# Kernel tuning notes

Measured on AMD Instinct MI355X. Metric: run time of the kernel, lower is better.

Reference implementation:

```python
import jax, jax.numpy as jnp
import numpy as np
import math

D_MODEL = 2048
K = 64
W = 512              # window_size
STRIDE = W // 2      # = 256
EMA_ALPHA = 0.9
N_RETRIEVE = 8
EPS = 1e-12


def _build_cheby(k, w):
    # cheby_mat[k, n] = cos(k * arccos(t_n)), t_n = cos(pi*(2n+1)/(2w))
    ns = np.arange(w, dtype=np.float64)
    t = np.cos(np.pi * (2 * ns + 1) / (2 * w))
    ks = np.arange(k, dtype=np.float64)
    return jnp.asarray(np.cos(ks[:, None] * np.arccos(t)[None, :]), dtype=jnp.float32)


def setup_inputs() -> dict:
    key = jax.random.key(0)
    ks = jax.random.split(key, 5)
    B, S = 2, 8192
    scan_out = jax.random.normal(ks[0], (B, S, D_MODEL), dtype=jnp.float32)
    buf = jax.random.normal(ks[1], (W, D_MODEL), dtype=jnp.float32)  # pre-filled circular buffer
    # unit-modulus random-phase complex roles: r_k[d] = exp(i*theta)
    phases = jax.random.uniform(ks[2], (K, D_MODEL), dtype=jnp.float32) * (2.0 * math.pi)
    roles_real = jnp.cos(phases)
    roles_imag = jnp.sin(phases)
    w_bands = 1.0 / (jnp.arange(K, dtype=jnp.float32) + 1.0)  # w_init = 1/(k+1)
    retrieve_proj_w = jax.random.normal(ks[3], (D_MODEL, D_MODEL), dtype=jnp.float32) * 0.02
    inject_gate = jnp.zeros((1,), dtype=jnp.float32)
    cheby_mat = _build_cheby(K, W)
    return dict(scan_out=scan_out, buf=buf, roles_real=roles_real, roles_imag=roles_imag,
                w_bands=w_bands, retrieve_proj_w=retrieve_proj_w, inject_gate=inject_gate,
                cheby_mat=cheby_mat)


def reference(scan_out, buf, roles_real, roles_imag, w_bands, retrieve_proj_w, inject_gate, cheby_mat):
    S = scan_out.shape[1]
    h_mean = scan_out.mean(axis=0)                      # [S, D] batch-mean like torch code
    n_chunks = S // STRIDE
    chunks = h_mean.reshape(n_chunks, STRIDE, D_MODEL)  # each chunk triggers one bind

    init = (buf, jnp.int32(0),
            jnp.zeros((K, D_MODEL), jnp.float32),   # c_past
            jnp.zeros((D_MODEL,), jnp.float32),     # V_mem_real
            jnp.zeros((D_MODEL,), jnp.float32),     # V_mem_imag
            jnp.zeros((K,), jnp.float32),           # _coeff_norms (EMA)
            jnp.zeros((K,), jnp.float32))           # spectral_delta

    def step(carry, chunk):
        b, pos, c_past, vr, vi, cnorms, _ = carry
        # circular-buffer write of `stride` tokens starting at pos
        b = jax.lax.dynamic_update_slice(b, chunk, (pos, 0))
        pos = (pos + STRIDE) % W
        order = (jnp.arange(W, dtype=jnp.int32) + pos) % W   # oldest-first reorder
        data = b[order]                                      # [W, D]
        # Chebyshev coefficients: c = (2/W) * cheby_mat @ data, c0 halved
        coeffs = (2.0 / W) * (cheby_mat @ data)              # [K, D]
        coeffs = coeffs.at[0].multiply(0.5)
        # HRR-normalized bind into holographic memory via EMA
        norms = jnp.maximum(jnp.linalg.norm(coeffs, axis=-1, keepdims=True), EPS)
        cn = coeffs / norms
        cnorms = EMA_ALPHA * cnorms + (1.0 - EMA_ALPHA) * norms[:, 0]
        vr = EMA_ALPHA * vr + (1.0 - EMA_ALPHA) * (cn * roles_real).sum(axis=0)
        vi = EMA_ALPHA * vi + (1.0 - EMA_ALPHA) * (cn * roles_imag).sum(axis=0)
        # spectral delta vs previous window's coefficients
        delta = jnp.linalg.norm(coeffs - c_past, axis=-1)    # [K]
        return (b, pos, coeffs, vr, vi, cnorms, delta), None

    (b, pos, c_now, vr, vi, cnorms, delta), _ = jax.lax.scan(step, init, chunks)

    # retrieve: unbind top-J bands by spectral delta, denormalize, weight, project
    _, top = jax.lax.top_k(delta, N_RETRIEVE)                # [J]
    rr = roles_real[top]
    ri = roles_imag[top]
    retrieved = (vr[None, :] * rr + vi[None, :] * ri) * jnp.maximum(cnorms[top], EPS)[:, None]  # [J, D]
    weights = jax.nn.softplus(w_bands[top])                  # [J]
    ctx = (weights[:, None] * retrieved).sum(axis=0)         # [D]
    out = (ctx @ retrieve_proj_w.T) * jax.nn.sigmoid(inject_gate[0])  # [D]
    return out, delta, vr, vi
```

## Files before the change

kernel.cpp:

```cpp
#include <hip/hip_runtime.h>
#include <math.h>

#define D_MODEL 2048
#define KB_ 64
#define NCHUNK 32

typedef __bf16 bf16;
typedef __attribute__((ext_vector_type(8))) __bf16 bf16x8;
typedef __attribute__((ext_vector_type(4))) __bf16 bf16x4;
typedef __attribute__((ext_vector_type(4))) float f32x4;

#define OFF_COEFFS 0
#define OFF_NSQ    (32 * 64 * 2048)
#define OFF_NORMS  (OFF_NSQ + 32 * 64 * 32)
#define OFF_PARTR  (OFF_NORMS + 2048)
#define OFF_PARTI  (OFF_PARTR + 32 * 2048)
#define OFF_CTX    (OFF_PARTI + 32 * 2048)
#define OFF_CHEB2  (OFF_CTX + 2048)

__global__ __launch_bounds__(256) void k0_prep(
    const float* __restrict__ cheby, bf16* __restrict__ cheb2)
{
  int flat = blockIdx.x * 256 + threadIdx.x;
  cheb2[flat] = (bf16)cheby[flat];
}

__global__ __launch_bounds__(256, 4) void k1_mfma(
    const float* __restrict__ scan, const float* __restrict__ buf,
    const bf16* __restrict__ cheb2, float* __restrict__ coeffs,
    float* __restrict__ nsq_part)
{
  __shared__ bf16 Bs[2][64 * 72];

  const int t = threadIdx.x;
  const int dt = blockIdx.x;
  const int c  = blockIdx.y;
  const int w = t >> 6, lane = t & 63;
  const int quad = lane >> 4, r16 = lane & 15;
  const int d0 = dt * 64;
  const int n0 = (t >> 4) * 4;
  const int d4 = (t & 15) * 4;
  const float* scan1 = scan + 8192 * 2048;

  f32x4 acc[4];
#pragma unroll
  for (int tn = 0; tn < 4; ++tn) acc[tn] = (f32x4){0.f, 0.f, 0.f, 0.f};

  float vv[4][4], vvn[4][4];

  auto loadB = [&](int nb, float (*v)[4]) {
    if (c == 0 && nb < 4) {
      const float* bp = buf + (256 + nb * 64 + n0) * 2048 + d0 + d4;
#pragma unroll
      for (int i = 0; i < 4; ++i) {
        float4 x = *(const float4*)(bp + i * 2048);
        v[i][0] = x.x; v[i][1] = x.y; v[i][2] = x.z; v[i][3] = x.w;
      }
    } else {
      int gbase = ((c - 1) * 256 + nb * 64 + n0) * 2048 + d0 + d4;
#pragma unroll
      for (int i = 0; i < 4; ++i) {
        float4 a = *(const float4*)(scan + gbase + i * 2048);
        float4 b = *(const float4*)(scan1 + gbase + i * 2048);
        v[i][0] = 0.5f * (a.x + b.x); v[i][1] = 0.5f * (a.y + b.y);
        v[i][2] = 0.5f * (a.z + b.z); v[i][3] = 0.5f * (a.w + b.w);
      }
    }
  };

  loadB(0, vv);
  for (int nb = 0; nb < 8; ++nb) {
    bf16* Bw = Bs[nb & 1];
#pragma unroll
    for (int x = 0; x < 4; ++x) {
      bf16x4 e = {(bf16)vv[0][x], (bf16)vv[1][x], (bf16)vv[2][x], (bf16)vv[3][x]};
      *(bf16x4*)(Bw + (d4 + x) * 72 + n0) = e;
    }
    __syncthreads();
    if (nb < 7) loadB(nb + 1, vvn);
    const bf16* abase = cheb2 + (w * 16 + r16) * 512 + nb * 64 + quad * 8;
    bf16x8 a0 = *(const bf16x8*)(abase);
    bf16x8 a1 = *(const bf16x8*)(abase + 32);
#pragma unroll
    for (int ks = 0; ks < 2; ++ks) {
      bf16x8 a = ks ? a1 : a0;
#pragma unroll
      for (int tn = 0; tn < 4; ++tn) {
        bf16x8 bfr = *(const bf16x8*)(Bw + (tn * 16 + r16) * 72 + ks * 32 + quad * 8);
        acc[tn] = __builtin_amdgcn_mfma_f32_16x16x32_bf16(a, bfr, acc[tn], 0, 0, 0);
      }
    }
#pragma unroll
    for (int i = 0; i < 4; ++i)
#pragma unroll
      for (int x = 0; x < 4; ++x) vv[i][x] = vvn[i][x];
  }

  const float scale = 2.0f / 512.0f;
  float sq[4] = {0.f, 0.f, 0.f, 0.f};
#pragma unroll
  for (int tn = 0; tn < 4; ++tn) {
#pragma unroll
    for (int rr = 0; rr < 4; ++rr) {
      int band = w * 16 + quad * 4 + rr;
      float sc = (band == 0) ? scale * 0.5f : scale;
      float v = acc[tn][rr] * sc;
      coeffs[(c * 64 + band) * 2048 + d0 + tn * 16 + r16] = v;
      sq[rr] += v * v;
    }
  }
#pragma unroll
  for (int off = 8; off > 0; off >>= 1) {
#pragma unroll
    for (int rr = 0; rr < 4; ++rr) sq[rr] += __shfl_down(sq[rr], off);
  }
  if (r16 == 0) {
#pragma unroll
    for (int rr = 0; rr < 4; ++rr)
      nsq_part[(c * 64 + w * 16 + quad * 4 + rr) * 32 + dt] = sq[rr];
  }
}

__global__ __launch_bounds__(256) void k3_bind(
    const float* __restrict__ coeffs, const float* __restrict__ nsq_part,
    const float* __restrict__ rr, const float* __restrict__ ri,
    float* __restrict__ part_r, float* __restrict__ part_i,
    float* __restrict__ norms, float* __restrict__ dout)
{
  const int tid = threadIdx.x;
  const int c = blockIdx.y;

  if (blockIdx.x == 2) {
    __shared__ float red[4];
#pragma unroll
    for (int kk = 0; kk < 2; ++kk) {
      int k = c + kk * 32;
      const float* p1 = coeffs + (31 * 64 + k) * 2048;
      const float* p0 = coeffs + (30 * 64 + k) * 2048;
      float s = 0.f;
#pragma unroll
      for (int i = 0; i < 2; ++i) {
        float4 a = *(const float4*)(p1 + tid * 4 + i * 1024);
        float4 b = *(const float4*)(p0 + tid * 4 + i * 1024);
        float x = a.x - b.x, y = a.y - b.y, z = a.z - b.z, ww = a.w - b.w;
        s += x * x + y * y + z * z + ww * ww;
      }
      for (int o = 32; o > 0; o >>= 1) s += __shfl_down(s, o, 64);
      if ((tid & 63) == 0) red[tid >> 6] = s;
      __syncthreads();
      if (tid == 0) dout[D_MODEL + k] = sqrtf(red[0] + red[1] + red[2] + red[3]);
      __syncthreads();
    }
    return;
  }

  __shared__ float inv_s[64];
  if (tid < 64) {
    float s = 0.f;
#pragma unroll
    for (int dtl = 0; dtl < 32; ++dtl) s += nsq_part[(c * 64 + tid) * 32 + dtl];
    float nrm = fmaxf(sqrtf(s), 1e-12f);
    inv_s[tid] = 1.0f / nrm;
    if (blockIdx.x == 0) norms[c * 64 + tid] = nrm;
  }
  __syncthreads();
  const int d4 = (blockIdx.x * 256 + tid) * 4;
  const float wc = 0.1f * powf(0.9f, (float)(31 - c));
  float4 ar = make_float4(0.f, 0.f, 0.f, 0.f);
  float4 ai = make_float4(0.f, 0.f, 0.f, 0.f);
  for (int k = 0; k < KB_; ++k) {
    float4 cf = *(const float4*)(coeffs + (c * 64 + k) * 2048 + d4);
    float inv = inv_s[k];
    float4 r = *(const float4*)(rr + k * D_MODEL + d4);
    float4 im = *(const float4*)(ri + k * D_MODEL + d4);
    float cx = cf.x * inv, cy = cf.y * inv, cz = cf.z * inv, cw = cf.w * inv;
    ar.x += cx * r.x; ar.y += cy * r.y; ar.z += cz * r.z; ar.w += cw * r.w;
    ai.x += cx * im.x; ai.y += cy * im.y; ai.z += cz * im.z; ai.w += cw * im.w;
  }
  *(float4*)(part_r + c * D_MODEL + d4) =
      make_float4(wc * ar.x, wc * ar.y, wc * ar.z, wc * ar.w);
  *(float4*)(part_i + c * D_MODEL + d4) =
      make_float4(wc * ai.x, wc * ai.y, wc * ai.z, wc * ai.w);
}

__global__ __launch_bounds__(256) void k4_ctx(
    const float* __restrict__ norms, const float* __restrict__ part_r,
    const float* __restrict__ part_i, const float* __restrict__ rr,
    const float* __restrict__ ri, const float* __restrict__ wbands,
    float* __restrict__ dout, float* __restrict__ ctx)
{
  __shared__ float cn_s[64];
  __shared__ int top_s[8];
  __shared__ float wgt_s[8];
  const int tid = threadIdx.x;
  const int d = blockIdx.x * 256 + tid;
  if (tid < 64) {
    float s = 0.f;
    for (int c = 0; c < NCHUNK; ++c) s = 0.9f * s + 0.1f * norms[c * 64 + tid];
    cn_s[tid] = fmaxf(s, 1e-12f);
  }
  __syncthreads();
  if (tid == 0) {
    unsigned long long taken = 0ULL;
    for (int jj = 0; jj < 8; ++jj) {
      float best = -1.f;
      int bi = 0;
      for (int k = 0; k < 64; ++k) {
        float dv = dout[D_MODEL + k];
        if (!((taken >> k) & 1ULL) && dv > best) { best = dv; bi = k; }
      }
      taken |= (1ULL << bi);
      top_s[jj] = bi;
      wgt_s[jj] = log1pf(expf(wbands[bi]));
    }
  }
  __syncthreads();
  float sr = 0.f, si = 0.f;
  for (int c = 0; c < NCHUNK; ++c) {
    sr += part_r[c * D_MODEL + d];
    si += part_i[c * D_MODEL + d];
  }
  dout[D_MODEL + KB_ + d] = sr;
  dout[D_MODEL + KB_ + D_MODEL + d] = si;
  float cx = 0.f;
#pragma unroll
  for (int jj = 0; jj < 8; ++jj) {
    int k = top_s[jj];
    cx += wgt_s[jj] * (sr * rr[k * D_MODEL + d] + si * ri[k * D_MODEL + d]) * cn_s[k];
  }
  ctx[d] = cx;
}

__global__ __launch_bounds__(256) void k5b_gemv(
    const float* __restrict__ Wp, const float* __restrict__ ctx,
    const float* __restrict__ gate, float* __restrict__ dout)
{
  const int tid = threadIdx.x;
  const int lane = tid & 63;
  const int w = tid >> 6;
  const int row = blockIdx.x * 4 + w;
  const float* p = Wp + row * D_MODEL;
  float s = 0.f;
#pragma unroll
  for (int i = 0; i < 8; ++i) {
    int e = lane * 4 + i * 256;
    float4 wv = *(const float4*)(p + e);
    float4 cv = *(const float4*)(ctx + e);
    s += wv.x * cv.x + wv.y * cv.y + wv.z * cv.z + wv.w * cv.w;
  }
  for (int o = 32; o > 0; o >>= 1) s += __shfl_down(s, o, 64);
  if (lane == 0) {
    float sig = 1.f / (1.f + expf(-gate[0]));
    dout[row] = s * sig;
  }
}

extern "C" void kernel_launch(void* const* d_in, const int* in_sizes, int n_in,
                              void* d_out, int out_size, void* d_ws, size_t ws_size,
                              hipStream_t stream) {
  const float* scan  = (const float*)d_in[0];
  const float* buf   = (const float*)d_in[1];
  const float* rr    = (const float*)d_in[2];
  const float* ri    = (const float*)d_in[3];
  const float* wb    = (const float*)d_in[4];
  const float* Wp    = (const float*)d_in[5];
  const float* gate  = (const float*)d_in[6];
  const float* cheby = (const float*)d_in[7];
  float* out = (float*)d_out;
  float* ws = (float*)d_ws;

  float* coeffs   = ws + OFF_COEFFS;
  float* nsq_part = ws + OFF_NSQ;
  float* norms    = ws + OFF_NORMS;
  float* part_r   = ws + OFF_PARTR;
  float* part_i   = ws + OFF_PARTI;
  float* ctx      = ws + OFF_CTX;
  bf16*  cheb2    = (bf16*)(ws + OFF_CHEB2);

  k0_prep<<<128, 256, 0, stream>>>(cheby, cheb2);
  k1_mfma<<<dim3(32, 32), 256, 0, stream>>>(scan, buf, cheb2, coeffs, nsq_part);
  k3_bind<<<dim3(3, NCHUNK), 256, 0, stream>>>(coeffs, nsq_part, rr, ri,
                                               part_r, part_i, norms, out);
  k4_ctx<<<8, 256, 0, stream>>>(norms, part_r, part_i, rr, ri, wb, out, ctx);
  k5b_gemv<<<512, 256, 0, stream>>>(Wp, ctx, gate, out);
}
```

Measured before the change: 321.5 us.

## Share overlapping window chunks across window pairs in Chebyshev MFMA kernel

Each block now computes two adjacent windows over a 32-wide d-tile. The overlapping 256-token half is loaded once and fed to both windows' accumulators, so global reads of scan (which are averaged across the batch) drop from 8 to 6 slices per window-pair half. The grid changes to 64x16, the nsq partials widen to 64 d-tiles, and the LDS double buffer is removed in favour of a single buffer with an extra barrier. The cost is less load/compute overlap and the loss of the explicit prefetch.

```diff
diff --git a/kernel.cpp b/kernel.cpp
--- a/kernel.cpp
+++ b/kernel.cpp
@@ -7,12 +7,12 @@
 
 typedef __bf16 bf16;
 typedef __attribute__((ext_vector_type(8))) __bf16 bf16x8;
-typedef __attribute__((ext_vector_type(4))) __bf16 bf16x4;
+typedef __attribute__((ext_vector_type(2))) __bf16 bf16x2;
 typedef __attribute__((ext_vector_type(4))) float f32x4;
 
 #define OFF_COEFFS 0
 #define OFF_NSQ    (32 * 64 * 2048)
-#define OFF_NORMS  (OFF_NSQ + 32 * 64 * 32)
+#define OFF_NORMS  (OFF_NSQ + 32 * 64 * 64)
 #define OFF_PARTR  (OFF_NORMS + 2048)
 #define OFF_PARTI  (OFF_PARTR + 32 * 2048)
 #define OFF_CTX    (OFF_PARTI + 32 * 2048)
@@ -25,99 +25,108 @@
   cheb2[flat] = (bf16)cheby[flat];
 }
 
-__global__ __launch_bounds__(256, 4) void k1_mfma(
+__global__ __launch_bounds__(256) void k1_mfma(
     const float* __restrict__ scan, const float* __restrict__ buf,
     const bf16* __restrict__ cheb2, float* __restrict__ coeffs,
     float* __restrict__ nsq_part)
 {
-  __shared__ bf16 Bs[2][64 * 72];
+  __shared__ bf16 Bs[32 * 72];
 
   const int t = threadIdx.x;
   const int dt = blockIdx.x;
-  const int c  = blockIdx.y;
+  const int p  = blockIdx.y;
   const int w = t >> 6, lane = t & 63;
   const int quad = lane >> 4, r16 = lane & 15;
-  const int d0 = dt * 64;
-  const int n0 = (t >> 4) * 4;
-  const int d4 = (t & 15) * 4;
+  const int d0 = dt * 32;
+  const int n0 = (t >> 3) * 2;
+  const int d4 = (t & 7) * 4;
   const float* scan1 = scan + 8192 * 2048;
 
-  f32x4 acc[4];
-#pragma unroll
-  for (int tn = 0; tn < 4; ++tn) acc[tn] = (f32x4){0.f, 0.f, 0.f, 0.f};
-
-  float vv[4][4], vvn[4][4];
-
-  auto loadB = [&](int nb, float (*v)[4]) {
-    if (c == 0 && nb < 4) {
-      const float* bp = buf + (256 + nb * 64 + n0) * 2048 + d0 + d4;
-#pragma unroll
-      for (int i = 0; i < 4; ++i) {
+  f32x4 acc[2][2];
+#pragma unroll
+  for (int a = 0; a < 2; ++a)
+#pragma unroll
+    for (int b = 0; b < 2; ++b) acc[a][b] = (f32x4){0.f, 0.f, 0.f, 0.f};
+
+  for (int sl = 0; sl < 12; ++sl) {
+    const int q = sl & 3;
+    float vv[2][4];
+    if (p == 0 && sl < 4) {
+      const float* bp = buf + (256 + sl * 64 + n0) * 2048 + d0 + d4;
+#pragma unroll
+      for (int i = 0; i < 2; ++i) {
         float4 x = *(const float4*)(bp + i * 2048);
-        v[i][0] = x.x; v[i][1] = x.y; v[i][2] = x.z; v[i][3] = x.w;
+        vv[i][0] = x.x; vv[i][1] = x.y; vv[i][2] = x.z; vv[i][3] = x.w;
       }
     } else {
-      int gbase = ((c - 1) * 256 + nb * 64 + n0) * 2048 + d0 + d4;
-#pragma unroll
-      for (int i = 0; i < 4; ++i) {
+      const int jc = 2 * p - 1 + (sl >> 2);
+      const int gbase = (jc * 256 + q * 64 + n0) * 2048 + d0 + d4;
+#pragma unroll
+      for (int i = 0; i < 2; ++i) {
         float4 a = *(const float4*)(scan + gbase + i * 2048);
         float4 b = *(const float4*)(scan1 + gbase + i * 2048);
-        v[i][0] = 0.5f * (a.x + b.x); v[i][1] = 0.5f * (a.y + b.y);
-        v[i][2] = 0.5f * (a.z + b.z); v[i][3] = 0.5f * (a.w + b.w);
-      }
-    }
-  };
-
-  loadB(0, vv);
-  for (int nb = 0; nb < 8; ++nb) {
-    bf16* Bw = Bs[nb & 1];
+        vv[i][0] = 0.5f * (a.x + b.x); vv[i][1] = 0.5f * (a.y + b.y);
+        vv[i][2] = 0.5f * (a.z + b.z); vv[i][3] = 0.5f * (a.w + b.w);
+      }
+    }
+    __syncthreads();
 #pragma unroll
     for (int x = 0; x < 4; ++x) {
-      bf16x4 e = {(bf16)vv[0][x], (bf16)vv[1][x], (bf16)vv[2][x], (bf16)vv[3][x]};
-      *(bf16x4*)(Bw + (d4 + x) * 72 + n0) = e;
+      bf16x2 e = {(bf16)vv[0][x], (bf16)vv[1][x]};
+      *(bf16x2*)(Bs + (d4 + x) * 72 + n0) = e;
     }
     __syncthreads();
-    if (nb < 7) loadB(nb + 1, vvn);
-    const bf16* abase = cheb2 + (w * 16 + r16) * 512 + nb * 64 + quad * 8;
-    bf16x8 a0 = *(const bf16x8*)(abase);
-    bf16x8 a1 = *(const bf16x8*)(abase + 32);
+
+    const bool wa = (sl < 8), wb = (sl >= 4);
+    const int colA = sl * 64, colB = (sl - 4) * 64;
+    const int arow = (w * 16 + r16) * 512;
 #pragma unroll
     for (int ks = 0; ks < 2; ++ks) {
-      bf16x8 a = ks ? a1 : a0;
-#pragma unroll
-      for (int tn = 0; tn < 4; ++tn) {
-        bf16x8 bfr = *(const bf16x8*)(Bw + (tn * 16 + r16) * 72 + ks * 32 + quad * 8);
-        acc[tn] = __builtin_amdgcn_mfma_f32_16x16x32_bf16(a, bfr, acc[tn], 0, 0, 0);
-      }
-    }
-#pragma unroll
-    for (int i = 0; i < 4; ++i)
-#pragma unroll
-      for (int x = 0; x < 4; ++x) vv[i][x] = vvn[i][x];
+      bf16x8 bfr[2];
+#pragma unroll
+      for (int tn = 0; tn < 2; ++tn)
+        bfr[tn] = *(const bf16x8*)(Bs + (tn * 16 + r16) * 72 + ks * 32 + quad * 8);
+      if (wa) {
+        bf16x8 a = *(const bf16x8*)(cheb2 + arow + colA + ks * 32 + quad * 8);
+#pragma unroll
+        for (int tn = 0; tn < 2; ++tn)
+          acc[0][tn] = __builtin_amdgcn_mfma_f32_16x16x32_bf16(a, bfr[tn], acc[0][tn], 0, 0, 0);
+      }
+      if (wb) {
+        bf16x8 a = *(const bf16x8*)(cheb2 + arow + colB + ks * 32 + quad * 8);
+#pragma unroll
+        for (int tn = 0; tn < 2; ++tn)
+          acc[1][tn] = __builtin_amdgcn_mfma_f32_16x16x32_bf16(a, bfr[tn], acc[1][tn], 0, 0, 0);
+      }
+    }
   }
 
   const float scale = 2.0f / 512.0f;
-  float sq[4] = {0.f, 0.f, 0.f, 0.f};
-#pragma unroll
-  for (int tn = 0; tn < 4; ++tn) {
-#pragma unroll
-    for (int rr = 0; rr < 4; ++rr) {
-      int band = w * 16 + quad * 4 + rr;
-      float sc = (band == 0) ? scale * 0.5f : scale;
-      float v = acc[tn][rr] * sc;
-      coeffs[(c * 64 + band) * 2048 + d0 + tn * 16 + r16] = v;
-      sq[rr] += v * v;
-    }
-  }
-#pragma unroll
-  for (int off = 8; off > 0; off >>= 1) {
-#pragma unroll
-    for (int rr = 0; rr < 4; ++rr) sq[rr] += __shfl_down(sq[rr], off);
-  }
-  if (r16 == 0) {
-#pragma unroll
-    for (int rr = 0; rr < 4; ++rr)
-      nsq_part[(c * 64 + w * 16 + quad * 4 + rr) * 32 + dt] = sq[rr];
+#pragma unroll
+  for (int win = 0; win < 2; ++win) {
+    const int c = 2 * p + win;
+    float sq[4] = {0.f, 0.f, 0.f, 0.f};
+#pragma unroll
+    for (int tn = 0; tn < 2; ++tn) {
+#pragma unroll
+      for (int rr = 0; rr < 4; ++rr) {
+        int band = w * 16 + quad * 4 + rr;
+        float sc = (band == 0) ? scale * 0.5f : scale;
+        float v = acc[win][tn][rr] * sc;
+        coeffs[(c * 64 + band) * 2048 + d0 + tn * 16 + r16] = v;
+        sq[rr] += v * v;
+      }
+    }
+#pragma unroll
+    for (int off = 8; off > 0; off >>= 1) {
+#pragma unroll
+      for (int rr = 0; rr < 4; ++rr) sq[rr] += __shfl_down(sq[rr], off);
+    }
+    if (r16 == 0) {
+#pragma unroll
+      for (int rr = 0; rr < 4; ++rr)
+        nsq_part[(c * 64 + w * 16 + quad * 4 + rr) * 64 + dt] = sq[rr];
+    }
   }
 }
 
@@ -158,7 +167,7 @@
   if (tid < 64) {
     float s = 0.f;
 #pragma unroll
-    for (int dtl = 0; dtl < 32; ++dtl) s += nsq_part[(c * 64 + tid) * 32 + dtl];
+    for (int dtl = 0; dtl < 64; ++dtl) s += nsq_part[(c * 64 + tid) * 64 + dtl];
     float nrm = fmaxf(sqrtf(s), 1e-12f);
     inv_s[tid] = 1.0f / nrm;
     if (blockIdx.x == 0) norms[c * 64 + tid] = nrm;
@@ -278,7 +287,7 @@
   bf16*  cheb2    = (bf16*)(ws + OFF_CHEB2);
 
   k0_prep<<<128, 256, 0, stream>>>(cheby, cheb2);
-  k1_mfma<<<dim3(32, 32), 256, 0, stream>>>(scan, buf, cheb2, coeffs, nsq_part);
+  k1_mfma<<<dim3(64, 16), 256, 0, stream>>>(scan, buf, cheb2, coeffs, nsq_part);
   k3_bind<<<dim3(3, NCHUNK), 256, 0, stream>>>(coeffs, nsq_part, rr, ri,
                                                part_r, part_i, norms, out);
   k4_ctx<<<8, 256, 0, stream>>>(norms, part_r, part_i, rr, ri, wb, out, ctx);
```

Result: no change. 322.5 us (+0.3%).

## Fuse all stages into one cooperative persistent kernel with grid syncs

Applied to the files above, without the earlier changes.

Adds a cooperative kernel that runs the bf16 conversion, the Chebyshev MFMA projection, the bind/delta reduction, the context build and the GEMV as phases separated by grid-wide syncs, launched with 512 blocks. The intent is to remove per-launch overhead and the gaps between the five kernels. The MFMA phase processes 1024 tiles in a grid-stride loop and drops the register double-buffering of the next B tile, so global load latency is no longer overlapped with compute. The fallback k1 kernel also loses its prefetch and its launch-bounds occupancy hint.

```diff
diff --git a/kernel.cpp b/kernel.cpp
--- a/kernel.cpp
+++ b/kernel.cpp
@@ -1,5 +1,8 @@
 #include <hip/hip_runtime.h>
+#include <hip/hip_cooperative_groups.h>
 #include <math.h>
+
+namespace cg = cooperative_groups;
 
 #define D_MODEL 2048
 #define KB_ 64
@@ -18,6 +21,229 @@
 #define OFF_CTX    (OFF_PARTI + 32 * 2048)
 #define OFF_CHEB2  (OFF_CTX + 2048)
 
+__global__ __launch_bounds__(256, 2) void fused_all(
+    const float* __restrict__ scan, const float* __restrict__ buf,
+    const float* __restrict__ rr, const float* __restrict__ ri,
+    const float* __restrict__ wbands, const float* __restrict__ Wp,
+    const float* __restrict__ gate, const float* __restrict__ cheby,
+    float* __restrict__ dout, float* __restrict__ coeffs,
+    float* __restrict__ nsq_part, float* __restrict__ norms,
+    float* __restrict__ part_r, float* __restrict__ part_i,
+    float* __restrict__ ctx, bf16* __restrict__ cheb2)
+{
+  cg::grid_group grid = cg::this_grid();
+  const int b = blockIdx.x;
+  const int tid = threadIdx.x;
+
+  __shared__ bf16 Bs[64 * 72];
+  __shared__ float sm64[64];
+  __shared__ float red[4];
+  __shared__ int top_s[8];
+  __shared__ float wgt_s[8];
+
+  if (b < 128) {
+    int flat = b * 256 + tid;
+    cheb2[flat] = (bf16)cheby[flat];
+  }
+  __threadfence();
+  grid.sync();
+
+  {
+    const int w = tid >> 6, lane = tid & 63;
+    const int quad = lane >> 4, r16 = lane & 15;
+    const int n0 = (tid >> 4) * 4;
+    const int d4s = (tid & 15) * 4;
+    const float* scan1 = scan + 8192 * 2048;
+
+    for (int tile = b; tile < 1024; tile += gridDim.x) {
+      const int dt = tile & 31;
+      const int c  = tile >> 5;
+      const int d0 = dt * 64;
+
+      f32x4 acc[4];
+#pragma unroll
+      for (int tn = 0; tn < 4; ++tn) acc[tn] = (f32x4){0.f, 0.f, 0.f, 0.f};
+
+      for (int nb = 0; nb < 8; ++nb) {
+        float vv[4][4];
+        if (c == 0 && nb < 4) {
+          const float* bp = buf + (256 + nb * 64 + n0) * 2048 + d0 + d4s;
+#pragma unroll
+          for (int i = 0; i < 4; ++i) {
+            float4 x = *(const float4*)(bp + i * 2048);
+            vv[i][0] = x.x; vv[i][1] = x.y; vv[i][2] = x.z; vv[i][3] = x.w;
+          }
+        } else {
+          int gbase = ((c - 1) * 256 + nb * 64 + n0) * 2048 + d0 + d4s;
+#pragma unroll
+          for (int i = 0; i < 4; ++i) {
+            float4 a = *(const float4*)(scan + gbase + i * 2048);
+            float4 bb = *(const float4*)(scan1 + gbase + i * 2048);
+            vv[i][0] = 0.5f * (a.x + bb.x); vv[i][1] = 0.5f * (a.y + bb.y);
+            vv[i][2] = 0.5f * (a.z + bb.z); vv[i][3] = 0.5f * (a.w + bb.w);
+          }
+        }
+        __syncthreads();
+#pragma unroll
+        for (int x = 0; x < 4; ++x) {
+          bf16x4 e = {(bf16)vv[0][x], (bf16)vv[1][x], (bf16)vv[2][x], (bf16)vv[3][x]};
+          *(bf16x4*)(Bs + (d4s + x) * 72 + n0) = e;
+        }
+        __syncthreads();
+
+        const bf16* abase = cheb2 + (w * 16 + r16) * 512 + nb * 64 + quad * 8;
+        bf16x8 a0 = *(const bf16x8*)(abase);
+        bf16x8 a1 = *(const bf16x8*)(abase + 32);
+#pragma unroll
+        for (int ks = 0; ks < 2; ++ks) {
+          bf16x8 a = ks ? a1 : a0;
+#pragma unroll
+          for (int tn = 0; tn < 4; ++tn) {
+            bf16x8 bfr = *(const bf16x8*)(Bs + (tn * 16 + r16) * 72 + ks * 32 + quad * 8);
+            acc[tn] = __builtin_amdgcn_mfma_f32_16x16x32_bf16(a, bfr, acc[tn], 0, 0, 0);
+          }
+        }
+      }
+
+      const float scale = 2.0f / 512.0f;
+      float sq[4] = {0.f, 0.f, 0.f, 0.f};
+#pragma unroll
+      for (int tn = 0; tn < 4; ++tn) {
+#pragma unroll
+        for (int r = 0; r < 4; ++r) {
+          int band = w * 16 + quad * 4 + r;
+          float sc = (band == 0) ? scale * 0.5f : scale;
+          float v = acc[tn][r] * sc;
+          coeffs[(c * 64 + band) * 2048 + d0 + tn * 16 + r16] = v;
+          sq[r] += v * v;
+        }
+      }
+#pragma unroll
+      for (int off = 8; off > 0; off >>= 1) {
+#pragma unroll
+        for (int r = 0; r < 4; ++r) sq[r] += __shfl_down(sq[r], off);
+      }
+      if (r16 == 0) {
+#pragma unroll
+        for (int r = 0; r < 4; ++r)
+          nsq_part[(c * 64 + w * 16 + quad * 4 + r) * 32 + dt] = sq[r];
+      }
+    }
+  }
+  __threadfence();
+  grid.sync();
+
+  if (b < 64) {
+    const int c = b >> 1;
+    const int half = b & 1;
+    if (tid < 64) {
+      float s = 0.f;
+#pragma unroll
+      for (int dtl = 0; dtl < 32; ++dtl) s += nsq_part[(c * 64 + tid) * 32 + dtl];
+      float nrm = fmaxf(sqrtf(s), 1e-12f);
+      sm64[tid] = 1.0f / nrm;
+      if (half == 0) norms[c * 64 + tid] = nrm;
+    }
+    __syncthreads();
+    const int d4 = (half * 256 + tid) * 4;
+    const float wc = 0.1f * powf(0.9f, (float)(31 - c));
+    float4 ar = make_float4(0.f, 0.f, 0.f, 0.f);
+    float4 ai = make_float4(0.f, 0.f, 0.f, 0.f);
+    for (int k = 0; k < KB_; ++k) {
+      float4 cf = *(const float4*)(coeffs + (c * 64 + k) * 2048 + d4);
+      float inv = sm64[k];
+      float4 r = *(const float4*)(rr + k * D_MODEL + d4);
+      float4 im = *(const float4*)(ri + k * D_MODEL + d4);
+      float cx = cf.x * inv, cy = cf.y * inv, cz = cf.z * inv, cw = cf.w * inv;
+      ar.x += cx * r.x; ar.y += cy * r.y; ar.z += cz * r.z; ar.w += cw * r.w;
+      ai.x += cx * im.x; ai.y += cy * im.y; ai.z += cz * im.z; ai.w += cw * im.w;
+    }
+    *(float4*)(part_r + c * D_MODEL + d4) =
+        make_float4(wc * ar.x, wc * ar.y, wc * ar.z, wc * ar.w);
+    *(float4*)(part_i + c * D_MODEL + d4) =
+        make_float4(wc * ai.x, wc * ai.y, wc * ai.z, wc * ai.w);
+  } else if (b < 128) {
+    const int k = b - 64;
+    const float* p1 = coeffs + (31 * 64 + k) * 2048;
+    const float* p0 = coeffs + (30 * 64 + k) * 2048;
+    float s = 0.f;
+#pragma unroll
+    for (int i = 0; i < 2; ++i) {
+      float4 a = *(const float4*)(p1 + tid * 4 + i * 1024);
+      float4 bb = *(const float4*)(p0 + tid * 4 + i * 1024);
+      float x = a.x - bb.x, y = a.y - bb.y, z = a.z - bb.z, ww = a.w - bb.w;
+      s += x * x + y * y + z * z + ww * ww;
+    }
+    for (int o = 32; o > 0; o >>= 1) s += __shfl_down(s, o, 64);
+    if ((tid & 63) == 0) red[tid >> 6] = s;
+    __syncthreads();
+    if (tid == 0) dout[D_MODEL + k] = sqrtf(red[0] + red[1] + red[2] + red[3]);
+  }
+  __threadfence();
+  grid.sync();
+
+  if (b < 8) {
+    const int d = b * 256 + tid;
+    if (tid < 64) {
+      float s = 0.f;
+      for (int c = 0; c < NCHUNK; ++c) s = 0.9f * s + 0.1f * norms[c * 64 + tid];
+      sm64[tid] = fmaxf(s, 1e-12f);
+    }
+    __syncthreads();
+    if (tid == 0) {
+      unsigned long long taken = 0ULL;
+      for (int jj = 0; jj < 8; ++jj) {
+        float best = -1.f;
+        int bi = 0;
+        for (int k = 0; k < 64; ++k) {
+          float dv = dout[D_MODEL + k];
+          if (!((taken >> k) & 1ULL) && dv > best) { best = dv; bi = k; }
+        }
+        taken |= (1ULL << bi);
+        top_s[jj] = bi;
+        wgt_s[jj] = log1pf(expf(wbands[bi]));
+      }
+    }
+    __syncthreads();
+    float sr = 0.f, si = 0.f;
+    for (int c = 0; c < NCHUNK; ++c) {
+      sr += part_r[c * D_MODEL + d];
+      si += part_i[c * D_MODEL + d];
+    }
+    dout[D_MODEL + KB_ + d] = sr;
+    dout[D_MODEL + KB_ + D_MODEL + d] = si;
+    float cx = 0.f;
+#pragma unroll
+    for (int jj = 0; jj < 8; ++jj) {
+      int k = top_s[jj];
+      cx += wgt_s[jj] * (sr * rr[k * D_MODEL + d] + si * ri[k * D_MODEL + d]) * sm64[k];
+    }
+    ctx[d] = cx;
+  }
+  __threadfence();
+  grid.sync();
+
+  {
+    const int lane = tid & 63;
+    const int w = tid >> 6;
+    const int row = b * 4 + w;
+    const float* p = Wp + row * D_MODEL;
+    float s = 0.f;
+#pragma unroll
+    for (int i = 0; i < 8; ++i) {
+      int e = lane * 4 + i * 256;
+      float4 wv = *(const float4*)(p + e);
+      float4 cv = *(const float4*)(ctx + e);
+      s += wv.x * cv.x + wv.y * cv.y + wv.z * cv.z + wv.w * cv.w;
+    }
+    for (int o = 32; o > 0; o >>= 1) s += __shfl_down(s, o, 64);
+    if (lane == 0) {
+      float sig = 1.f / (1.f + expf(-gate[0]));
+      dout[row] = s * sig;
+    }
+  }
+}
+
 __global__ __launch_bounds__(256) void k0_prep(
     const float* __restrict__ cheby, bf16* __restrict__ cheb2)
 {
@@ -25,59 +251,51 @@
   cheb2[flat] = (bf16)cheby[flat];
 }
 
-__global__ __launch_bounds__(256, 4) void k1_mfma(
+__global__ __launch_bounds__(256) void k1_mfma(
     const float* __restrict__ scan, const float* __restrict__ buf,
     const bf16* __restrict__ cheb2, float* __restrict__ coeffs,
     float* __restrict__ nsq_part)
 {
-  __shared__ bf16 Bs[2][64 * 72];
-
+  __shared__ bf16 Bs[64 * 72];
   const int t = threadIdx.x;
-  const int dt = blockIdx.x;
-  const int c  = blockIdx.y;
+  const int dt = blockIdx.x, c = blockIdx.y;
   const int w = t >> 6, lane = t & 63;
   const int quad = lane >> 4, r16 = lane & 15;
   const int d0 = dt * 64;
   const int n0 = (t >> 4) * 4;
-  const int d4 = (t & 15) * 4;
+  const int d4s = (t & 15) * 4;
   const float* scan1 = scan + 8192 * 2048;
 
   f32x4 acc[4];
 #pragma unroll
   for (int tn = 0; tn < 4; ++tn) acc[tn] = (f32x4){0.f, 0.f, 0.f, 0.f};
 
-  float vv[4][4], vvn[4][4];
-
-  auto loadB = [&](int nb, float (*v)[4]) {
+  for (int nb = 0; nb < 8; ++nb) {
+    float vv[4][4];
     if (c == 0 && nb < 4) {
-      const float* bp = buf + (256 + nb * 64 + n0) * 2048 + d0 + d4;
+      const float* bp = buf + (256 + nb * 64 + n0) * 2048 + d0 + d4s;
 #pragma unroll
       for (int i = 0; i < 4; ++i) {
         float4 x = *(const float4*)(bp + i * 2048);
-        v[i][0] = x.x; v[i][1] = x.y; v[i][2] = x.z; v[i][3] = x.w;
+        vv[i][0] = x.x; vv[i][1] = x.y; vv[i][2] = x.z; vv[i][3] = x.w;
       }
     } else {
-      int gbase = ((c - 1) * 256 + nb * 64 + n0) * 2048 + d0 + d4;
+      int gbase = ((c - 1) * 256 + nb * 64 + n0) * 2048 + d0 + d4s;
 #pragma unroll
       for (int i = 0; i < 4; ++i) {
         float4 a = *(const float4*)(scan + gbase + i * 2048);
-        float4 b = *(const float4*)(scan1 + gbase + i * 2048);
-        v[i][0] = 0.5f * (a.x + b.x); v[i][1] = 0.5f * (a.y + b.y);
-        v[i][2] = 0.5f * (a.z + b.z); v[i][3] = 0.5f * (a.w + b.w);
-      }
-    }
-  };
-
-  loadB(0, vv);
-  for (int nb = 0; nb < 8; ++nb) {
-    bf16* Bw = Bs[nb & 1];
+        float4 bb = *(const float4*)(scan1 + gbase + i * 2048);
+        vv[i][0] = 0.5f * (a.x + bb.x); vv[i][1] = 0.5f * (a.y + bb.y);
+        vv[i][2] = 0.5f * (a.z + bb.z); vv[i][3] = 0.5f * (a.w + bb.w);
+      }
+    }
+    __syncthreads();
 #pragma unroll
     for (int x = 0; x < 4; ++x) {
       bf16x4 e = {(bf16)vv[0][x], (bf16)vv[1][x], (bf16)vv[2][x], (bf16)vv[3][x]};
-      *(bf16x4*)(Bw + (d4 + x) * 72 + n0) = e;
+      *(bf16x4*)(Bs + (d4s + x) * 72 + n0) = e;
     }
     __syncthreads();
-    if (nb < 7) loadB(nb + 1, vvn);
     const bf16* abase = cheb2 + (w * 16 + r16) * 512 + nb * 64 + quad * 8;
     bf16x8 a0 = *(const bf16x8*)(abase);
     bf16x8 a1 = *(const bf16x8*)(abase + 32);
@@ -86,14 +304,10 @@
       bf16x8 a = ks ? a1 : a0;
 #pragma unroll
       for (int tn = 0; tn < 4; ++tn) {
-        bf16x8 bfr = *(const bf16x8*)(Bw + (tn * 16 + r16) * 72 + ks * 32 + quad * 8);
+        bf16x8 bfr = *(const bf16x8*)(Bs + (tn * 16 + r16) * 72 + ks * 32 + quad * 8);
         acc[tn] = __builtin_amdgcn_mfma_f32_16x16x32_bf16(a, bfr, acc[tn], 0, 0, 0);
       }
     }
-#pragma unroll
-    for (int i = 0; i < 4; ++i)
-#pragma unroll
-      for (int x = 0; x < 4; ++x) vv[i][x] = vvn[i][x];
   }
 
   const float scale = 2.0f / 512.0f;
@@ -101,23 +315,23 @@
 #pragma unroll
   for (int tn = 0; tn < 4; ++tn) {
 #pragma unroll
-    for (int rr = 0; rr < 4; ++rr) {
-      int band = w * 16 + quad * 4 + rr;
+    for (int r = 0; r < 4; ++r) {
+      int band = w * 16 + quad * 4 + r;
       float sc = (band == 0) ? scale * 0.5f : scale;
-      float v = acc[tn][rr] * sc;
+      float v = acc[tn][r] * sc;
       coeffs[(c * 64 + band) * 2048 + d0 + tn * 16 + r16] = v;
-      sq[rr] += v * v;
+      sq[r] += v * v;
     }
   }
 #pragma unroll
   for (int off = 8; off > 0; off >>= 1) {
 #pragma unroll
-    for (int rr = 0; rr < 4; ++rr) sq[rr] += __shfl_down(sq[rr], off);
+    for (int r = 0; r < 4; ++r) sq[r] += __shfl_down(sq[r], off);
   }
   if (r16 == 0) {
 #pragma unroll
-    for (int rr = 0; rr < 4; ++rr)
-      nsq_part[(c * 64 + w * 16 + quad * 4 + rr) * 32 + dt] = sq[rr];
+    for (int r = 0; r < 4; ++r)
+      nsq_part[(c * 64 + w * 16 + quad * 4 + r) * 32 + dt] = sq[r];
   }
 }
 
@@ -129,7 +343,6 @@
 {
   const int tid = threadIdx.x;
   const int c = blockIdx.y;
-
   if (blockIdx.x == 2) {
     __shared__ float red[4];
 #pragma unroll
@@ -153,7 +366,6 @@
     }
     return;
   }
-
   __shared__ float inv_s[64];
   if (tid < 64) {
     float s = 0.f;
@@ -277,6 +489,23 @@
   float* ctx      = ws + OFF_CTX;
   bf16*  cheb2    = (bf16*)(ws + OFF_CHEB2);
 
+  int maxB = 0;
+  hipError_t qerr = hipOccupancyMaxActiveBlocksPerMultiprocessor(
+      &maxB, fused_all, 256, 0);
+  bool coop_ok = (qerr == hipSuccess && maxB >= 2);
+
+  if (coop_ok) {
+    void* args[] = {
+      (void*)&scan, (void*)&buf, (void*)&rr, (void*)&ri, (void*)&wb,
+      (void*)&Wp, (void*)&gate, (void*)&cheby, (void*)&out,
+      (void*)&coeffs, (void*)&nsq_part, (void*)&norms,
+      (void*)&part_r, (void*)&part_i, (void*)&ctx, (void*)&cheb2
+    };
+    hipError_t lerr = hipLaunchCooperativeKernel(
+        (const void*)fused_all, dim3(512), dim3(256), args, 0, stream);
+    if (lerr == hipSuccess) return;
+  }
+
   k0_prep<<<128, 256, 0, stream>>>(cheby, cheb2);
   k1_mfma<<<dim3(32, 32), 256, 0, stream>>>(scan, buf, cheb2, coeffs, nsq_part);
   k3_bind<<<dim3(3, NCHUNK), 256, 0, stream>>>(coeffs, nsq_part, rr, ri,
```

Result: slower. 643.9 us (+100.3%).
